# Performance work log

Measured on AMD Instinct MI355X. Metric: run time of the kernel, lower is better.

## Reference

```python
import jax, jax.numpy as jnp
import numpy as np

D = 8           # spatial size of conv feature map
K = 24          # conv channels
Q = 128         # question embedding size
IN_SIZE = 2 * (K + 2) + Q  # 180
HID = 256
OUT = 28


def _coords(d):
    # faithful to torch float-tensor arithmetic: a/d is float division
    a = jnp.arange(d * d, dtype=jnp.float32)
    cx = (a / d - d / 2) / (d / 2.0)
    cy = (a % d - d / 2) / (d / 2.0)
    return jnp.stack([cx, cy], axis=1)  # [d^2, 2]


def setup_inputs() -> dict:
    key = jax.random.key(0)
    ks = jax.random.split(key, 16)
    s = 0.05
    inp = {
        "x": jax.random.normal(ks[0], (64, K, D, D), dtype=jnp.float32),
        "qst": jax.random.normal(ks[1], (64, Q), dtype=jnp.float32),
        # g MLP (weights stored [in, out])
        "g1_w": jax.random.normal(ks[2], (IN_SIZE, HID), dtype=jnp.float32) * s,
        "g1_b": jnp.zeros((HID,), dtype=jnp.float32),
        "g2_w": jax.random.normal(ks[3], (HID, HID), dtype=jnp.float32) * s,
        "g2_b": jnp.zeros((HID,), dtype=jnp.float32),
        "g3_w": jax.random.normal(ks[4], (HID, HID), dtype=jnp.float32) * s,
        "g3_b": jnp.zeros((HID,), dtype=jnp.float32),
        "g4_w": jax.random.normal(ks[5], (HID, HID), dtype=jnp.float32) * s,
        "g4_b": jnp.zeros((HID,), dtype=jnp.float32),
        # f MLP
        "f1_w": jax.random.normal(ks[6], (HID, HID), dtype=jnp.float32) * s,
        "f1_b": jnp.zeros((HID,), dtype=jnp.float32),
        "f2_w": jax.random.normal(ks[7], (HID, HID), dtype=jnp.float32) * s,
        "f2_b": jnp.zeros((HID,), dtype=jnp.float32),
        "f3_w": jax.random.normal(ks[8], (HID, OUT), dtype=jnp.float32) * s,
        "f3_b": jnp.zeros((OUT,), dtype=jnp.float32),
    }
    return inp


def _forward(x, qst, g1_w, g1_b, g2_w, g2_b, g3_w, g3_b, g4_w, g4_b,
             f1_w, f1_b, f2_w, f2_b, f3_w, f3_b):
    b, k, d, _ = x.shape
    n = d * d  # 64 objects
    # [b, n, k] object features + 2 coord channels -> [b, n, 26]
    xf = jnp.transpose(x.reshape(b, k, n), (0, 2, 1))
    ct = jnp.broadcast_to(_coords(d)[None], (b, n, 2))
    xf = jnp.concatenate([xf, ct], axis=2)                      # [b, n, 26]
    obj = k + 2
    # x_i: varies along axis 2 (original torch layout); x_j varies along axis 1 and carries qst
    xi = jnp.broadcast_to(xf[:, None, :, :], (b, n, n, obj))
    xjq = jnp.concatenate(
        [xf, jnp.broadcast_to(qst[:, None, :], (b, n, qst.shape[1]))], axis=2)
    xj = jnp.broadcast_to(xjq[:, :, None, :], (b, n, n, obj + qst.shape[1]))
    pair = jnp.concatenate([xi, xj], axis=3)                    # [b, n, n, 180]
    # g MLP over all pairs
    h = jax.nn.relu(pair @ g1_w + g1_b)
    h = jax.nn.relu(h @ g2_w + g2_b)
    h = jax.nn.relu(h @ g3_w + g3_b)
    h = jax.nn.relu(h @ g4_w + g4_b)                            # [b, n, n, 256]
    xg = jnp.sum(h, axis=(1, 2))                                # sum over d^4 pairs
    # f MLP (dropout is identity in eval mode)
    xf_ = jax.nn.relu(xg @ f1_w + f1_b)
    xf_ = jax.nn.relu(xf_ @ f2_w + f2_b)
    logits = xf_ @ f3_w + f3_b
    return jax.nn.log_softmax(logits, axis=-1)


def reference(x, qst, g1_w, g1_b, g2_w, g2_b, g3_w, g3_b, g4_w, g4_b,
              f1_w, f1_b, f2_w, f2_b, f3_w, f3_b):
    return _forward(x, qst, g1_w, g1_b, g2_w, g2_b, g3_w, g3_b, g4_w, g4_b,
                    f1_w, f1_b, f2_w, f2_b, f3_w, f3_b)
```

## Files before the change

### kernel.cpp

```cpp
#include <hip/hip_runtime.h>

typedef __bf16 bf16_t;
typedef __bf16 bf16x8 __attribute__((ext_vector_type(8)));
typedef __bf16 bf16x4 __attribute__((ext_vector_type(4)));
typedef float  f32x4  __attribute__((ext_vector_type(4)));


__global__ __launch_bounds__(256) void rn_prep_kernel(
    const float* __restrict__ x, const float* __restrict__ qst,
    const float* __restrict__ g1w, const float* __restrict__ g1b,
    const float* __restrict__ g2w, const float* __restrict__ g3w,
    const float* __restrict__ g4w,
    float* __restrict__ A, float* __restrict__ C,
    bf16_t* __restrict__ Wt)
{
  __shared__ float T[64][65];
  int blk = blockIdx.x;
  int n   = threadIdx.x;
  if (blk < 256) {
    int b  = blk >> 2;
    int jg = (blk & 3) * 16;
    float accQ = g1b[n];
    const float* qb = qst + b * 128;
    #pragma unroll 8
    for (int qi = 0; qi < 128; ++qi)
      accQ += qb[qi] * g1w[(52 + qi) * 256 + n];

    float w24 = g1w[24 * 256 + n], w25 = g1w[25 * 256 + n];
    float w50 = g1w[50 * 256 + n], w51 = g1w[51 * 256 + n];
    float accA[16], accC[16];
    #pragma unroll
    for (int t = 0; t < 16; ++t) {
      int j = jg + t;
      float cx = ((float)j * 0.125f - 4.0f) * 0.25f;
      float cy = ((float)(j & 7) - 4.0f) * 0.25f;
      accA[t] = cx * w24 + cy * w25;
      accC[t] = accQ + cx * w50 + cy * w51;
    }
    for (int c = 0; c < 24; ++c) {
      float wa = g1w[c * 256 + n];
      float wc = g1w[(26 + c) * 256 + n];
      const float* xc = x + (b * 24 + c) * 64 + jg;
      #pragma unroll
      for (int t = 0; t < 16; ++t) {
        float xv = xc[t];
        accA[t] += xv * wa;
        accC[t] += xv * wc;
      }
    }
    #pragma unroll
    for (int t = 0; t < 16; ++t) {
      A[(b * 64 + jg + t) * 256 + n] = accA[t];
      C[(b * 64 + jg + t) * 256 + n] = accC[t];
    }
  } else {
    int t   = blk - 256;
    int mat = t >> 4;
    int tl  = t & 15;
    int kt  = (tl & 3) * 64;
    int nt_ = (tl >> 2) * 64;
    const float* W = (mat == 0) ? g2w : (mat == 1 ? g3w : g4w);
    int lane = n & 63, w = n >> 6;
    #pragma unroll
    for (int it = 0; it < 16; ++it) {
      int kl = w * 16 + it;
      T[kl][lane] = W[(kt + kl) * 256 + nt_ + lane];
    }
    __syncthreads();
    #pragma unroll
    for (int it = 0; it < 16; ++it) {
      int nl  = w * 16 + it;
      int no  = nt_ + nl;
      int k   = kt + lane;
      int tile = no >> 4, rr = no & 15;
      int ksI  = k >> 5,  qI = (k >> 3) & 3, e = k & 7;
      int idx  = ((tile * 8 + ksI) * 64 + qI * 16 + rr) * 8 + e;
      Wt[mat * 65536 + idx] = (bf16_t)T[lane][nl];
    }
  }
}

__global__ __launch_bounds__(256, 4) void rn_main_kernel(
    const float* __restrict__ A, const float* __restrict__ C,
    const bf16_t* __restrict__ Wt,
    const float* __restrict__ g2b, const float* __restrict__ g3b,
    const float* __restrict__ g4b,
    float* __restrict__ part)
{
  __shared__ bf16_t h[16384];

  int tid  = threadIdx.x;
  int bx0  = blockIdx.x;
  int bx   = (bx0 & 7) * 512 + (bx0 >> 3);
  int b    = bx >> 6;
  int i    = bx & 63;
  int lane = tid & 63;
  int wave = tid >> 6;
  int r    = lane & 15;
  int q    = lane >> 4;

  {
    const float* Ab = A + (size_t)b * 64 * 256;
    const float* Cr = C + ((size_t)b * 64 + i) * 256;
    int j = wave * 16 + r;
    #pragma unroll
    for (int it = 0; it < 8; ++it) {
      int k0 = it * 32 + q * 8;
      const float4 a0 = *(const float4*)(Ab + j * 256 + k0);
      const float4 a1 = *(const float4*)(Ab + j * 256 + k0 + 4);
      const float4 c0 = *(const float4*)(Cr + k0);
      const float4 c1 = *(const float4*)(Cr + k0 + 4);
      bf16x8 v;
      v[0] = (bf16_t)fmaxf(a0.x + c0.x, 0.f);
      v[1] = (bf16_t)fmaxf(a0.y + c0.y, 0.f);
      v[2] = (bf16_t)fmaxf(a0.z + c0.z, 0.f);
      v[3] = (bf16_t)fmaxf(a0.w + c0.w, 0.f);
      v[4] = (bf16_t)fmaxf(a1.x + c1.x, 0.f);
      v[5] = (bf16_t)fmaxf(a1.y + c1.y, 0.f);
      v[6] = (bf16_t)fmaxf(a1.z + c1.z, 0.f);
      v[7] = (bf16_t)fmaxf(a1.w + c1.w, 0.f);
      *(bf16x8*)&h[((wave * 8 + it) * 64 + lane) * 8] = v;
    }
  }

  for (int L = 0; L < 3; ++L) {
    __syncthreads();
    const bf16_t* Wl   = Wt + L * 65536 + wave * 16384;
    const float*  bias = (L == 0) ? g2b : (L == 1) ? g3b : g4b;

    f32x4 acc[4][4];
    #pragma unroll
    for (int nt = 0; nt < 4; ++nt)
      #pragma unroll
      for (int mt = 0; mt < 4; ++mt)
        #pragma unroll
        for (int e = 0; e < 4; ++e) acc[nt][mt][e] = 0.f;

    #pragma unroll
    for (int ks = 0; ks < 8; ++ks) {
      bf16x8 wf[4], hf[4];
      #pragma unroll
      for (int nt = 0; nt < 4; ++nt)
        wf[nt] = *(const bf16x8*)&Wl[((nt * 8 + ks) * 64 + lane) * 8];
      #pragma unroll
      for (int mt = 0; mt < 4; ++mt)
        hf[mt] = *(const bf16x8*)&h[((mt * 8 + ks) * 64 + lane) * 8];
      #pragma unroll
      for (int nt = 0; nt < 4; ++nt)
        #pragma unroll
        for (int mt = 0; mt < 4; ++mt)
          acc[nt][mt] = __builtin_amdgcn_mfma_f32_16x16x32_bf16(
              wf[nt], hf[mt], acc[nt][mt], 0, 0, 0);
    }

    __syncthreads();

    if (L < 2) {
      #pragma unroll
      for (int nt = 0; nt < 4; ++nt) {
        int k0  = wave * 64 + nt * 16 + q * 4;
        float4 bv = *(const float4*)&bias[k0];
        int ks_ = k0 >> 5, rem = k0 & 31;
        int qp  = rem >> 3, e0 = rem & 7;
        #pragma unroll
        for (int mt = 0; mt < 4; ++mt) {
          bf16x4 v;
          v[0] = (bf16_t)fmaxf(acc[nt][mt][0] + bv.x, 0.f);
          v[1] = (bf16_t)fmaxf(acc[nt][mt][1] + bv.y, 0.f);
          v[2] = (bf16_t)fmaxf(acc[nt][mt][2] + bv.z, 0.f);
          v[3] = (bf16_t)fmaxf(acc[nt][mt][3] + bv.w, 0.f);
          int off = ((mt * 8 + ks_) * 64 + qp * 16 + r) * 8 + e0;
          *(bf16x4*)&h[off] = v;
        }
      }
    } else {
      #pragma unroll
      for (int nt = 0; nt < 4; ++nt) {
        int k0 = wave * 64 + nt * 16 + q * 4;
        float4 bv = *(const float4*)&bias[k0];
        float p0 = 0.f, p1 = 0.f, p2 = 0.f, p3 = 0.f;
        #pragma unroll
        for (int mt = 0; mt < 4; ++mt) {
          p0 += fmaxf(acc[nt][mt][0] + bv.x, 0.f);
          p1 += fmaxf(acc[nt][mt][1] + bv.y, 0.f);
          p2 += fmaxf(acc[nt][mt][2] + bv.z, 0.f);
          p3 += fmaxf(acc[nt][mt][3] + bv.w, 0.f);
        }
        #pragma unroll
        for (int d = 1; d < 16; d <<= 1) {
          p0 += __shfl_xor(p0, d, 64);
          p1 += __shfl_xor(p1, d, 64);
          p2 += __shfl_xor(p2, d, 64);
          p3 += __shfl_xor(p3, d, 64);
        }
        if (r == 0) {
          float4 pv = make_float4(p0, p1, p2, p3);
          *(float4*)&part[(size_t)bx * 256 + k0] = pv;
        }
      }
    }
  }
}

__global__ __launch_bounds__(256) void rn_f_kernel(
    const float* __restrict__ part,
    const float* __restrict__ f1w, const float* __restrict__ f1b,
    const float* __restrict__ f2w, const float* __restrict__ f2b,
    const float* __restrict__ f3w, const float* __restrict__ f3b,
    float* __restrict__ out)
{
  __shared__ float xs[256], t1[256], t2[256], lg[28], lse[1];
  int b = blockIdx.x, tid = threadIdx.x;
  float s = 0.f;
  const float* pb = part + (size_t)b * 64 * 256;
  #pragma unroll 8
  for (int i = 0; i < 64; ++i) s += pb[i * 256 + tid];
  xs[tid] = s;
  __syncthreads();
  float acc = f1b[tid];
  for (int k = 0; k < 256; ++k) acc += xs[k] * f1w[k * 256 + tid];
  t1[tid] = fmaxf(acc, 0.f);
  __syncthreads();
  acc = f2b[tid];
  for (int k = 0; k < 256; ++k) acc += t1[k] * f2w[k * 256 + tid];
  t2[tid] = fmaxf(acc, 0.f);
  __syncthreads();
  if (tid < 28) {
    float a2 = f3b[tid];
    for (int k = 0; k < 256; ++k) a2 += t2[k] * f3w[k * 28 + tid];
    lg[tid] = a2;
  }
  __syncthreads();
  if (tid == 0) {
    float m = lg[0];
    for (int j = 1; j < 28; ++j) m = fmaxf(m, lg[j]);
    float se = 0.f;
    for (int j = 0; j < 28; ++j) se += expf(lg[j] - m);
    lse[0] = m + logf(se);
  }
  __syncthreads();
  if (tid < 28) out[b * 28 + tid] = lg[tid] - lse[0];
}

extern "C" void kernel_launch(void* const* d_in, const int* in_sizes, int n_in,
                              void* d_out, int out_size, void* d_ws, size_t ws_size,
                              hipStream_t stream) {
  (void)in_sizes; (void)n_in; (void)out_size; (void)ws_size;
  const float* x   = (const float*)d_in[0];
  const float* qst = (const float*)d_in[1];
  const float* g1w = (const float*)d_in[2];
  const float* g1b = (const float*)d_in[3];
  const float* g2w = (const float*)d_in[4];
  const float* g2b = (const float*)d_in[5];
  const float* g3w = (const float*)d_in[6];
  const float* g3b = (const float*)d_in[7];
  const float* g4w = (const float*)d_in[8];
  const float* g4b = (const float*)d_in[9];
  const float* f1w = (const float*)d_in[10];
  const float* f1b = (const float*)d_in[11];
  const float* f2w = (const float*)d_in[12];
  const float* f2b = (const float*)d_in[13];
  const float* f3w = (const float*)d_in[14];
  const float* f3b = (const float*)d_in[15];
  float* out = (float*)d_out;

  float*  A    = (float*)d_ws;
  float*  C    = A + 4096 * 256;
  bf16_t* Wt   = (bf16_t*)(C + 4096 * 256);
  float*  part = (float*)((char*)Wt + 3 * 65536 * sizeof(bf16_t));

  rn_prep_kernel<<<256 + 48, 256, 0, stream>>>(
      x, qst, g1w, g1b, g2w, g3w, g4w, A, C, Wt);
  rn_main_kernel<<<4096, 256, 0, stream>>>(A, C, Wt, g2b, g3b, g4b, part);
  rn_f_kernel<<<64, 256, 0, stream>>>(part, f1w, f1b, f2w, f2b, f3w, f3b, out);
}
```

Baseline: 252.3 us.

## Switch g-MLP to 32x32x16 MFMA with 128-row tiles per block

Each block of the main kernel now handles 128 pair rows (two i values) instead of 64, using 32x32x16 bf16 MFMA tiles with a re-laid-out weight format. The aim is to reuse each weight fragment across more rows and to issue fewer, larger MFMAs. It also raises wave priority around the MFMA burst. In exchange, LDS per block doubles, occupancy drops to 2 blocks per CU, and the accumulator register footprint grows.

New measurement: 248.5 us. About the same (-1.5%).

```diff
diff --git a/kernel.cpp b/kernel.cpp
--- a/kernel.cpp
+++ b/kernel.cpp
@@ -4,6 +4,7 @@
 typedef __bf16 bf16x8 __attribute__((ext_vector_type(8)));
 typedef __bf16 bf16x4 __attribute__((ext_vector_type(4)));
 typedef float  f32x4  __attribute__((ext_vector_type(4)));
+typedef float  f32x16 __attribute__((ext_vector_type(16)));
 
 
 __global__ __launch_bounds__(256) void rn_prep_kernel(
@@ -72,42 +73,41 @@
       int nl  = w * 16 + it;
       int no  = nt_ + nl;
       int k   = kt + lane;
-      int tile = no >> 4, rr = no & 15;
-      int ksI  = k >> 5,  qI = (k >> 3) & 3, e = k & 7;
-      int idx  = ((tile * 8 + ksI) * 64 + qI * 16 + rr) * 8 + e;
+      int tile = no >> 5, r5 = no & 31;
+      int ksI  = k >> 4, hi = (k >> 3) & 1, e = k & 7;
+      int idx  = ((tile * 16 + ksI) * 64 + hi * 32 + r5) * 8 + e;
       Wt[mat * 65536 + idx] = (bf16_t)T[lane][nl];
     }
   }
 }
 
-__global__ __launch_bounds__(256, 4) void rn_main_kernel(
+__global__ __launch_bounds__(256, 2) void rn_main_kernel(
     const float* __restrict__ A, const float* __restrict__ C,
     const bf16_t* __restrict__ Wt,
     const float* __restrict__ g2b, const float* __restrict__ g3b,
     const float* __restrict__ g4b,
     float* __restrict__ part)
 {
-  __shared__ bf16_t h[16384];
+  __shared__ bf16_t h[32768];
 
   int tid  = threadIdx.x;
   int bx0  = blockIdx.x;
-  int bx   = (bx0 & 7) * 512 + (bx0 >> 3);
-  int b    = bx >> 6;
-  int i    = bx & 63;
+  int bx   = (bx0 & 7) * 256 + (bx0 >> 3);
+  int b    = bx >> 5;
+  int ip   = bx & 31;
   int lane = tid & 63;
   int wave = tid >> 6;
-  int r    = lane & 15;
-  int q    = lane >> 4;
+  int c5   = lane & 31;
+  int hi5  = lane >> 5;
 
   {
-    const float* Ab = A + (size_t)b * 64 * 256;
-    const float* Cr = C + ((size_t)b * 64 + i) * 256;
-    int j = wave * 16 + r;
-    #pragma unroll
-    for (int it = 0; it < 8; ++it) {
-      int k0 = it * 32 + q * 8;
-      const float4 a0 = *(const float4*)(Ab + j * 256 + k0);
-      const float4 a1 = *(const float4*)(Ab + j * 256 + k0 + 4);
+    const float* Ar = A + ((size_t)b * 64 + ((wave & 1) * 32 + c5)) * 256;
+    const float* Cr = C + ((size_t)b * 64 + ip * 2 + (wave >> 1)) * 256;
+    #pragma unroll
+    for (int it = 0; it < 16; ++it) {
+      int k0 = it * 16 + hi5 * 8;
+      const float4 a0 = *(const float4*)(Ar + k0);
+      const float4 a1 = *(const float4*)(Ar + k0 + 4);
       const float4 c0 = *(const float4*)(Cr + k0);
       const float4 c1 = *(const float4*)(Cr + k0 + 4);
       bf16x8 v;
@@ -119,83 +119,92 @@
       v[5] = (bf16_t)fmaxf(a1.y + c1.y, 0.f);
       v[6] = (bf16_t)fmaxf(a1.z + c1.z, 0.f);
       v[7] = (bf16_t)fmaxf(a1.w + c1.w, 0.f);
-      *(bf16x8*)&h[((wave * 8 + it) * 64 + lane) * 8] = v;
+      *(bf16x8*)&h[((wave * 16 + it) * 64 + lane) * 8] = v;
     }
   }
 
   for (int L = 0; L < 3; ++L) {
     __syncthreads();
-    const bf16_t* Wl   = Wt + L * 65536 + wave * 16384;
+    const bf16_t* Wl   = Wt + L * 65536;
     const float*  bias = (L == 0) ? g2b : (L == 1) ? g3b : g4b;
 
-    f32x4 acc[4][4];
-    #pragma unroll
-    for (int nt = 0; nt < 4; ++nt)
+    f32x16 acc[2][4];
+    #pragma unroll
+    for (int nt = 0; nt < 2; ++nt)
       #pragma unroll
       for (int mt = 0; mt < 4; ++mt)
         #pragma unroll
-        for (int e = 0; e < 4; ++e) acc[nt][mt][e] = 0.f;
-
-    #pragma unroll
-    for (int ks = 0; ks < 8; ++ks) {
-      bf16x8 wf[4], hf[4];
-      #pragma unroll
-      for (int nt = 0; nt < 4; ++nt)
-        wf[nt] = *(const bf16x8*)&Wl[((nt * 8 + ks) * 64 + lane) * 8];
+        for (int e = 0; e < 16; ++e) acc[nt][mt][e] = 0.f;
+
+    #pragma unroll
+    for (int ks = 0; ks < 16; ++ks) {
+      bf16x8 wf[2], hf[4];
+      #pragma unroll
+      for (int nt = 0; nt < 2; ++nt) {
+        int tile = wave * 2 + nt;
+        wf[nt] = *(const bf16x8*)&Wl[((tile * 16 + ks) * 64 + lane) * 8];
+      }
       #pragma unroll
       for (int mt = 0; mt < 4; ++mt)
-        hf[mt] = *(const bf16x8*)&h[((mt * 8 + ks) * 64 + lane) * 8];
-      #pragma unroll
-      for (int nt = 0; nt < 4; ++nt)
+        hf[mt] = *(const bf16x8*)&h[((mt * 16 + ks) * 64 + lane) * 8];
+      __builtin_amdgcn_s_setprio(1);
+      #pragma unroll
+      for (int nt = 0; nt < 2; ++nt)
         #pragma unroll
         for (int mt = 0; mt < 4; ++mt)
-          acc[nt][mt] = __builtin_amdgcn_mfma_f32_16x16x32_bf16(
+          acc[nt][mt] = __builtin_amdgcn_mfma_f32_32x32x16_bf16(
               wf[nt], hf[mt], acc[nt][mt], 0, 0, 0);
+      __builtin_amdgcn_s_setprio(0);
     }
 
     __syncthreads();
 
     if (L < 2) {
       #pragma unroll
-      for (int nt = 0; nt < 4; ++nt) {
-        int k0  = wave * 64 + nt * 16 + q * 4;
-        float4 bv = *(const float4*)&bias[k0];
-        int ks_ = k0 >> 5, rem = k0 & 31;
-        int qp  = rem >> 3, e0 = rem & 7;
-        #pragma unroll
-        for (int mt = 0; mt < 4; ++mt) {
-          bf16x4 v;
-          v[0] = (bf16_t)fmaxf(acc[nt][mt][0] + bv.x, 0.f);
-          v[1] = (bf16_t)fmaxf(acc[nt][mt][1] + bv.y, 0.f);
-          v[2] = (bf16_t)fmaxf(acc[nt][mt][2] + bv.z, 0.f);
-          v[3] = (bf16_t)fmaxf(acc[nt][mt][3] + bv.w, 0.f);
-          int off = ((mt * 8 + ks_) * 64 + qp * 16 + r) * 8 + e0;
-          *(bf16x4*)&h[off] = v;
+      for (int nt = 0; nt < 2; ++nt) {
+        #pragma unroll
+        for (int a = 0; a < 4; ++a) {
+          int nb = wave * 64 + nt * 32 + 4 * hi5 + 8 * (a & 1) + 16 * (a >> 1);
+          float4 bv = *(const float4*)&bias[nb];
+          int ksp = wave * 4 + nt * 2 + (a >> 1);
+          #pragma unroll
+          for (int mt = 0; mt < 4; ++mt) {
+            bf16x4 v;
+            v[0] = (bf16_t)fmaxf(acc[nt][mt][a * 4 + 0] + bv.x, 0.f);
+            v[1] = (bf16_t)fmaxf(acc[nt][mt][a * 4 + 1] + bv.y, 0.f);
+            v[2] = (bf16_t)fmaxf(acc[nt][mt][a * 4 + 2] + bv.z, 0.f);
+            v[3] = (bf16_t)fmaxf(acc[nt][mt][a * 4 + 3] + bv.w, 0.f);
+            int off = ((mt * 16 + ksp) * 64 + (a & 1) * 32 + c5) * 8 + 4 * hi5;
+            *(bf16x4*)&h[off] = v;
+          }
         }
       }
     } else {
       #pragma unroll
-      for (int nt = 0; nt < 4; ++nt) {
-        int k0 = wave * 64 + nt * 16 + q * 4;
-        float4 bv = *(const float4*)&bias[k0];
-        float p0 = 0.f, p1 = 0.f, p2 = 0.f, p3 = 0.f;
-        #pragma unroll
-        for (int mt = 0; mt < 4; ++mt) {
-          p0 += fmaxf(acc[nt][mt][0] + bv.x, 0.f);
-          p1 += fmaxf(acc[nt][mt][1] + bv.y, 0.f);
-          p2 += fmaxf(acc[nt][mt][2] + bv.z, 0.f);
-          p3 += fmaxf(acc[nt][mt][3] + bv.w, 0.f);
-        }
-        #pragma unroll
-        for (int d = 1; d < 16; d <<= 1) {
-          p0 += __shfl_xor(p0, d, 64);
-          p1 += __shfl_xor(p1, d, 64);
-          p2 += __shfl_xor(p2, d, 64);
-          p3 += __shfl_xor(p3, d, 64);
-        }
-        if (r == 0) {
-          float4 pv = make_float4(p0, p1, p2, p3);
-          *(float4*)&part[(size_t)bx * 256 + k0] = pv;
+      for (int nt = 0; nt < 2; ++nt) {
+        #pragma unroll
+        for (int a = 0; a < 4; ++a) {
+          int nb = wave * 64 + nt * 32 + 4 * hi5 + 8 * (a & 1) + 16 * (a >> 1);
+          float4 bv = *(const float4*)&bias[nb];
+          float p0 = 0.f, p1 = 0.f, p2 = 0.f, p3 = 0.f;
+          #pragma unroll
+          for (int mt = 0; mt < 4; ++mt) {
+            p0 += fmaxf(acc[nt][mt][a * 4 + 0] + bv.x, 0.f);
+            p1 += fmaxf(acc[nt][mt][a * 4 + 1] + bv.y, 0.f);
+            p2 += fmaxf(acc[nt][mt][a * 4 + 2] + bv.z, 0.f);
+            p3 += fmaxf(acc[nt][mt][a * 4 + 3] + bv.w, 0.f);
+          }
+          #pragma unroll
+          for (int d = 1; d < 32; d <<= 1) {
+            p0 += __shfl_xor(p0, d, 64);
+            p1 += __shfl_xor(p1, d, 64);
+            p2 += __shfl_xor(p2, d, 64);
+            p3 += __shfl_xor(p3, d, 64);
+          }
+          if (c5 == 0) {
+            float4 pv = make_float4(p0, p1, p2, p3);
+            *(float4*)&part[(size_t)bx * 256 + nb] = pv;
+          }
         }
       }
     }
@@ -212,9 +221,9 @@
   __shared__ float xs[256], t1[256], t2[256], lg[28], lse[1];
   int b = blockIdx.x, tid = threadIdx.x;
   float s = 0.f;
-  const float* pb = part + (size_t)b * 64 * 256;
+  const float* pb = part + (size_t)b * 32 * 256;
   #pragma unroll 8
-  for (int i = 0; i < 64; ++i) s += pb[i * 256 + tid];
+  for (int i = 0; i < 32; ++i) s += pb[i * 256 + tid];
   xs[tid] = s;
   __syncthreads();
   float acc = f1b[tid];
@@ -271,6 +280,6 @@
 
   rn_prep_kernel<<<256 + 48, 256, 0, stream>>>(
       x, qst, g1w, g1b, g2w, g3w, g4w, A, C, Wt);
-  rn_main_kernel<<<4096, 256, 0, stream>>>(A, C, Wt, g2b, g3b, g4b, part);
+  rn_main_kernel<<<2048, 256, 0, stream>>>(A, C, Wt, g2b, g3b, g4b, part);
   rn_f_kernel<<<64, 256, 0, stream>>>(part, f1w, f1b, f2w, f2b, f3w, f3b, out);
 }
```

## Double-buffer LDS activations, pre-layout A for coalesced loads, raise MFMA priority

Applied to the files above, without the earlier changes.

The prep kernel now writes the A term in a layout matching the main kernel's MFMA fragment order, so each lane reads contiguous floats. The main kernel ping-pongs hidden activations between two LDS buffers, which removes one of the two barriers per layer, and wraps the MFMA bursts in s_setprio. LDS use doubles to 64 KB per block and launch bounds drop from 4 to 2 blocks per CU, which may reduce occupancy and latency hiding.

Result: faster. 229.4 us (-9.1%).

```diff
diff --git a/kernel.cpp b/kernel.cpp
--- a/kernel.cpp
+++ b/kernel.cpp
@@ -11,7 +11,7 @@
     const float* __restrict__ g1w, const float* __restrict__ g1b,
     const float* __restrict__ g2w, const float* __restrict__ g3w,
     const float* __restrict__ g4w,
-    float* __restrict__ A, float* __restrict__ C,
+    float* __restrict__ Ap, float* __restrict__ C,
     bf16_t* __restrict__ Wt)
 {
   __shared__ float T[64][65];
@@ -48,9 +48,12 @@
         accC[t] += xv * wc;
       }
     }
+    int jt = blk & 3;
+    int itA = n >> 5, qA = (n >> 3) & 3, eA = n & 7;
+    int baseA = b * 16384 + (jt * 8 + itA) * 512 + qA * 128 + eA;
     #pragma unroll
     for (int t = 0; t < 16; ++t) {
-      A[(b * 64 + jg + t) * 256 + n] = accA[t];
+      Ap[baseA + t * 8] = accA[t];
       C[(b * 64 + jg + t) * 256 + n] = accC[t];
     }
   } else {
@@ -80,14 +83,15 @@
   }
 }
 
-__global__ __launch_bounds__(256, 4) void rn_main_kernel(
-    const float* __restrict__ A, const float* __restrict__ C,
+__global__ __launch_bounds__(256, 2) void rn_main_kernel(
+    const float* __restrict__ Ap, const float* __restrict__ C,
     const bf16_t* __restrict__ Wt,
     const float* __restrict__ g2b, const float* __restrict__ g3b,
     const float* __restrict__ g4b,
     float* __restrict__ part)
 {
-  __shared__ bf16_t h[16384];
+  __shared__ bf16_t hA[16384];
+  __shared__ bf16_t hB[16384];
 
   int tid  = threadIdx.x;
   int bx0  = blockIdx.x;
@@ -100,14 +104,13 @@
   int q    = lane >> 4;
 
   {
-    const float* Ab = A + (size_t)b * 64 * 256;
-    const float* Cr = C + ((size_t)b * 64 + i) * 256;
-    int j = wave * 16 + r;
+    const float* Apb = Ap + (size_t)b * 16384 + wave * 4096;
+    const float* Cr  = C + ((size_t)b * 64 + i) * 256;
     #pragma unroll
     for (int it = 0; it < 8; ++it) {
       int k0 = it * 32 + q * 8;
-      const float4 a0 = *(const float4*)(Ab + j * 256 + k0);
-      const float4 a1 = *(const float4*)(Ab + j * 256 + k0 + 4);
+      const float4 a0 = *(const float4*)(Apb + it * 512 + lane * 8);
+      const float4 a1 = *(const float4*)(Apb + it * 512 + lane * 8 + 4);
       const float4 c0 = *(const float4*)(Cr + k0);
       const float4 c1 = *(const float4*)(Cr + k0 + 4);
       bf16x8 v;
@@ -119,12 +122,15 @@
       v[5] = (bf16_t)fmaxf(a1.y + c1.y, 0.f);
       v[6] = (bf16_t)fmaxf(a1.z + c1.z, 0.f);
       v[7] = (bf16_t)fmaxf(a1.w + c1.w, 0.f);
-      *(bf16x8*)&h[((wave * 8 + it) * 64 + lane) * 8] = v;
-    }
-  }
-
+      *(bf16x8*)&hA[((wave * 8 + it) * 64 + lane) * 8] = v;
+    }
+  }
+  __syncthreads();
+
+  #pragma unroll
   for (int L = 0; L < 3; ++L) {
-    __syncthreads();
+    const bf16_t* hs = (L == 1) ? hB : hA;
+    bf16_t*       hd = (L == 0) ? hB : hA;
     const bf16_t* Wl   = Wt + L * 65536 + wave * 16384;
     const float*  bias = (L == 0) ? g2b : (L == 1) ? g3b : g4b;
 
@@ -144,16 +150,16 @@
         wf[nt] = *(const bf16x8*)&Wl[((nt * 8 + ks) * 64 + lane) * 8];
       #pragma unroll
       for (int mt = 0; mt < 4; ++mt)
-        hf[mt] = *(const bf16x8*)&h[((mt * 8 + ks) * 64 + lane) * 8];
+        hf[mt] = *(const bf16x8*)&hs[((mt * 8 + ks) * 64 + lane) * 8];
+      __builtin_amdgcn_s_setprio(1);
       #pragma unroll
       for (int nt = 0; nt < 4; ++nt)
         #pragma unroll
         for (int mt = 0; mt < 4; ++mt)
           acc[nt][mt] = __builtin_amdgcn_mfma_f32_16x16x32_bf16(
               wf[nt], hf[mt], acc[nt][mt], 0, 0, 0);
-    }
-
-    __syncthreads();
+      __builtin_amdgcn_s_setprio(0);
+    }
 
     if (L < 2) {
       #pragma unroll
@@ -170,9 +176,10 @@
           v[2] = (bf16_t)fmaxf(acc[nt][mt][2] + bv.z, 0.f);
           v[3] = (bf16_t)fmaxf(acc[nt][mt][3] + bv.w, 0.f);
           int off = ((mt * 8 + ks_) * 64 + qp * 16 + r) * 8 + e0;
-          *(bf16x4*)&h[off] = v;
+          *(bf16x4*)&hd[off] = v;
         }
       }
+      __syncthreads();
     } else {
       #pragma unroll
       for (int nt = 0; nt < 4; ++nt) {
@@ -264,13 +271,13 @@
   const float* f3b = (const float*)d_in[15];
   float* out = (float*)d_out;
 
-  float*  A    = (float*)d_ws;
-  float*  C    = A + 4096 * 256;
+  float*  Ap   = (float*)d_ws;
+  float*  C    = Ap + 4096 * 256;
   bf16_t* Wt   = (bf16_t*)(C + 4096 * 256);
   float*  part = (float*)((char*)Wt + 3 * 65536 * sizeof(bf16_t));
 
   rn_prep_kernel<<<256 + 48, 256, 0, stream>>>(
-      x, qst, g1w, g1b, g2w, g3w, g4w, A, C, Wt);
-  rn_main_kernel<<<4096, 256, 0, stream>>>(A, C, Wt, g2b, g3b, g4b, part);
+      x, qst, g1w, g1b, g2w, g3w, g4w, Ap, C, Wt);
+  rn_main_kernel<<<4096, 256, 0, stream>>>(Ap, C, Wt, g2b, g3b, g4b, part);
   rn_f_kernel<<<64, 256, 0, stream>>>(part, f1w, f1b, f2w, f2b, f3w, f3b, out);
 }
```
